# Performance work log

Hardware: AMD Instinct MI355X
Metric: run time of the kernel (lower is better)

The kernel has to match this reference:

```python
import jax, jax.numpy as jnp
import numpy as np

NUM_QUBITS = 512
NUM_CORES = 16
CORE_SIZE = 64
HIDDEN = 128
BATCH = 2048


def setup_inputs() -> dict:
    key = jax.random.key(0)
    k1, k2, k3 = jax.random.split(key, 3)
    last_assignment = jax.random.randint(k1, (BATCH, NUM_QUBITS), 0, NUM_CORES, dtype=jnp.int32)
    adjacency = jnp.ones((NUM_CORES, NUM_CORES), dtype=jnp.float32)  # all-to-all core graph
    qubit_embedding = jax.random.normal(k2, (NUM_QUBITS + 1, HIDDEN), dtype=jnp.float32)
    gcn_weight = jax.random.normal(k3, (HIDDEN, HIDDEN), dtype=jnp.float32) * (1.0 / np.sqrt(HIDDEN))
    gcn_bias = jnp.zeros((HIDDEN,), dtype=jnp.float32)
    return {
        'last_assignment': last_assignment,
        'adjacency': adjacency,
        'qubit_embedding': qubit_embedding,
        'gcn_weight': gcn_weight,
        'gcn_bias': gcn_bias,
    }


def reference(last_assignment, adjacency, qubit_embedding, gcn_weight, gcn_bias):
    B, Q = last_assignment.shape
    C = adjacency.shape[0]
    # --- replace the sequential per-qubit scatter loop with a single cumsum ---
    # pos[b,q] = number of earlier qubits assigned to the same core (the loop's
    # running counter idx); core index C (the extra row) always writes slot 0
    # because the loop resets its counter every iteration.
    oh = jax.nn.one_hot(last_assignment, C + 1, dtype=jnp.int32)        # [B,Q,C+1]
    cnt = jnp.cumsum(oh, axis=1)                                        # inclusive counts
    pos = jnp.take_along_axis(cnt, last_assignment[..., None], axis=2)[..., 0] - 1
    pos = jnp.where(last_assignment == C, 0, pos)
    buf = jnp.full((B, C + 1, CORE_SIZE), Q, dtype=jnp.int32)           # padding id = num_qubits
    b_idx = jnp.arange(B)[:, None]
    q_idx = jnp.broadcast_to(jnp.arange(Q, dtype=jnp.int32)[None, :], (B, Q))
    buf = buf.at[b_idx, last_assignment, pos].set(q_idx, mode='drop')
    buf = buf[:, :C, :]                                                 # drop overflow core row
    # --- embedding (padding row forced to zero, as nn.Embedding padding_idx) ---
    tbl = qubit_embedding.at[Q].set(0.0)
    qubit_embs = tbl[buf]                                               # [B,C,core_size,H]
    core_embs = qubit_embs.max(axis=2)                                  # [B,C,H]
    # --- GCNConv(add_self_loops=False): D^{-1/2} A D^{-1/2} (X W^T) + b ---
    deg = adjacency.sum(axis=0)
    dinv = jnp.where(deg > 0, 1.0 / jnp.sqrt(deg), 0.0)
    a_norm = adjacency * dinv[:, None] * dinv[None, :]                  # symmetric norm
    h = jnp.einsum('bch,oh->bco', core_embs, gcn_weight)                # lin (PyG: x @ W^T)
    out = jnp.einsum('ij,bjo->bio', a_norm, h) + gcn_bias               # [B,C,H]
    return out
```

## Files before the change

kernel.cpp:

```cpp
#include <hip/hip_runtime.h>
#include <stdint.h>

typedef unsigned short u16;
typedef unsigned int u32;
typedef unsigned long long u64;

typedef __bf16 bf16x8 __attribute__((ext_vector_type(8)));
typedef float f32x4 __attribute__((ext_vector_type(4)));
typedef u16 u16x8 __attribute__((ext_vector_type(8)));

#define NQ 512
#define NC 16
#define NH 128
#define NB 2048
#define ESTRIDE 136
#define HSTRIDE 24
#define QE_KEYS (513*128)
#define WT_OFF  QE_KEYS
#define GW_ELEMS (128*128)

static __device__ __forceinline__ u16 f2bf_rne(float f){
  u32 u = __float_as_uint(f);
  u += 0x7fffu + ((u>>16)&1u);
  return (u16)(u>>16);
}
static __device__ __forceinline__ u32 pack_rne(float lo, float hi){
  return (u32)f2bf_rne(lo) | ((u32)f2bf_rne(hi)<<16);
}
static __device__ __forceinline__ u16 key_of(float f){
  u16 b = f2bf_rne(f);
  return (b & 0x8000u) ? (u16)~b : (u16)(b | 0x8000u);
}
static __device__ __forceinline__ u16 unkey(u16 k){
  return (k & 0x8000u) ? (u16)(k ^ 0x8000u) : (u16)~k;
}

union Frag { u32 u[4]; uint4 u4; bf16x8 f; };
union U8   { u16x8 v; int w[4]; uint4 u4; u16 h[8]; };

__global__ void prepass_kernel(const float* __restrict__ qe,
                               const float* __restrict__ gw,
                               u16* __restrict__ ws)
{
  int idx = blockIdx.x * 256 + threadIdx.x;
  if (idx < QE_KEYS/8) {
    int i8 = idx * 8;
    uint4 o;
    if (i8 >= 512*NH) {
      o.x = 0x80008000u; o.y = 0x80008000u; o.z = 0x80008000u; o.w = 0x80008000u;
    } else {
      const float4* p = (const float4*)(qe + i8);
      float4 a = p[0], b = p[1];
      o.x = (u32)key_of(a.x) | ((u32)key_of(a.y)<<16);
      o.y = (u32)key_of(a.z) | ((u32)key_of(a.w)<<16);
      o.z = (u32)key_of(b.x) | ((u32)key_of(b.y)<<16);
      o.w = (u32)key_of(b.z) | ((u32)key_of(b.w)<<16);
    }
    *(uint4*)(ws + i8) = o;
  } else if (idx < QE_KEYS/8 + GW_ELEMS/8) {
    int j8 = (idx - QE_KEYS/8) * 8;
    const float4* p = (const float4*)(gw + j8);
    float4 a = p[0], b = p[1];
    uint4 o;
    o.x = pack_rne(a.x, a.y); o.y = pack_rne(a.z, a.w);
    o.z = pack_rne(b.x, b.y); o.w = pack_rne(b.z, b.w);
    *(uint4*)(ws + WT_OFF + j8) = o;
  }
}

__global__ __launch_bounds__(256, 8)
void core_snapshot_kernel(const int* __restrict__ la,
                          const float* __restrict__ adj,
                          const u16* __restrict__ ws,
                          const float* __restrict__ gb,
                          float* __restrict__ outp)
{
  __shared__ __align__(16) u16 sE[16*ESTRIDE];
  __shared__ __align__(16) u16 sHB[128*HSTRIDE];
  __shared__ u16 sList[16*64];
  __shared__ u32 sHist[8*16];
  __shared__ u32 sBase[8*16];
  __shared__ u32 sCnt[16];
  __shared__ float sDinv[16];

  const int tid  = threadIdx.x;
  const int lane = tid & 63;
  const int wv   = tid >> 6;
  const int m    = lane & 15;
  const int quad = lane >> 4;
  const int b    = blockIdx.x;
  const u16* qt  = ws;
  const u16* wt  = ws + WT_OFF;

  int av[2]; u32 intra[2];
  const u64 lmask = (1ull << lane) - 1ull;
  #pragma unroll
  for (int r = 0; r < 2; ++r) {
    int ch = wv*2 + r;
    av[r] = la[b*NQ + ch*64 + lane];
  }
  #pragma unroll
  for (int r = 0; r < 2; ++r) {
    int ch = wv*2 + r;
    #pragma unroll
    for (int c = 0; c < 16; ++c) {
      u64 mk = __ballot(av[r] == c);
      if (lane == c)  sHist[ch*16 + c] = (u32)__popcll(mk);
      if (av[r] == c) intra[r] = (u32)__popcll(mk & lmask);
    }
  }
  if (tid < 16) {
    float s = 0.f;
    for (int i = 0; i < 16; ++i) s += adj[i*16 + tid];
    sDinv[tid] = (s > 0.f) ? (1.0f / sqrtf(s)) : 0.f;
  }
  __syncthreads();
  if (tid < 16) {
    u32 run = 0;
    #pragma unroll
    for (int ch = 0; ch < 8; ++ch) { sBase[ch*16 + tid] = run; run += sHist[ch*16 + tid]; }
    sCnt[tid] = run;
  }
  __syncthreads();
  #pragma unroll
  for (int r = 0; r < 2; ++r) {
    int ch = wv*2 + r;
    u32 rank = sBase[ch*16 + av[r]] + intra[r];
    if (rank < 64) sList[av[r]*64 + rank] = (u16)(ch*64 + lane);
  }
  __syncthreads();

  for (int cc = 0; cc < 4; ++cc) {
    int c = wv*4 + cc;
    int cntc = (int)min(sCnt[c], 64u);
    U8 A; A.v = (u16x8)0;
    int iters = (cntc + 3) >> 2;
    for (int k = 0; k < iters; ++k) {
      int slot = k*4 + quad;
      int qv = (slot < cntc) ? (int)sList[c*64 + slot] : 512;
      U8 T; T.u4 = *(const uint4*)(qt + qv*NH + m*8);
      A.v = __builtin_elementwise_max(A.v, T.v);
    }
    U8 Bv;
    #pragma unroll
    for (int j = 0; j < 4; ++j) Bv.w[j] = __shfl_xor(A.w[j], 16);
    A.v = __builtin_elementwise_max(A.v, Bv.v);
    #pragma unroll
    for (int j = 0; j < 4; ++j) Bv.w[j] = __shfl_xor(A.w[j], 32);
    A.v = __builtin_elementwise_max(A.v, Bv.v);
    if (cntc < 64) {
      U8 Z; Z.v = (u16x8)(u16)0x8000u;
      A.v = __builtin_elementwise_max(A.v, Z.v);
    }
    if (quad == 0) {
      uint4 e;
      e.x = (u32)unkey(A.h[0]) | ((u32)unkey(A.h[1])<<16);
      e.y = (u32)unkey(A.h[2]) | ((u32)unkey(A.h[3])<<16);
      e.z = (u32)unkey(A.h[4]) | ((u32)unkey(A.h[5])<<16);
      e.w = (u32)unkey(A.h[6]) | ((u32)unkey(A.h[7])<<16);
      *(uint4*)&sE[c*ESTRIDE + m*8] = e;
    }
  }
  __syncthreads();

  {
    bf16x8 af[4];
    #pragma unroll
    for (int ks = 0; ks < 4; ++ks)
      af[ks] = *(const bf16x8*)&sE[m*ESTRIDE + ks*32 + quad*8];
    #pragma unroll
    for (int t = 0; t < 2; ++t) {
      int o = (wv*2 + t)*16 + m;
      f32x4 acc = {0.f, 0.f, 0.f, 0.f};
      #pragma unroll
      for (int ks = 0; ks < 4; ++ks) {
        bf16x8 bfr = *(const bf16x8*)(wt + o*NH + ks*32 + quad*8);
        acc = __builtin_amdgcn_mfma_f32_16x16x32_bf16(af[ks], bfr, acc, 0, 0, 0);
      }
      *(u32*)&sHB[o*HSTRIDE + quad*4]     = pack_rne(acc[0], acc[1]);
      *(u32*)&sHB[o*HSTRIDE + quad*4 + 2] = pack_rne(acc[2], acc[3]);
    }
  }
  __syncthreads();

  Frag afr2;
  #pragma unroll
  for (int jj = 0; jj < 4; ++jj) {
    float lo = 0.f, hi = 0.f;
    if (quad < 2) {
      int k0 = quad*8 + jj*2;
      lo = adj[m*16 + k0]     * sDinv[m] * sDinv[k0];
      hi = adj[m*16 + k0 + 1] * sDinv[m] * sDinv[k0 + 1];
    }
    afr2.u[jj] = pack_rne(lo, hi);
  }
  #pragma unroll
  for (int t = 0; t < 2; ++t) {
    int o = (wv*2 + t)*16 + m;
    float biasv = gb[(wv*2 + t)*16 + m];
    Frag bfr;
    if (quad < 2) bfr.u4 = *(const uint4*)&sHB[o*HSTRIDE + quad*8];
    else { bfr.u[0]=0; bfr.u[1]=0; bfr.u[2]=0; bfr.u[3]=0; }
    f32x4 acc = {biasv, biasv, biasv, biasv};
    acc = __builtin_amdgcn_mfma_f32_16x16x32_bf16(afr2.f, bfr.f, acc, 0, 0, 0);
    float* op = outp + b*(NC*NH) + o;
    #pragma unroll
    for (int r = 0; r < 4; ++r) op[(quad*4 + r)*NH] = acc[r];
  }
}

extern "C" void kernel_launch(void* const* d_in, const int* in_sizes, int n_in,
                              void* d_out, int out_size, void* d_ws, size_t ws_size,
                              hipStream_t stream) {
  const int*   la  = (const int*)d_in[0];
  const float* adj = (const float*)d_in[1];
  const float* qe  = (const float*)d_in[2];
  const float* gw  = (const float*)d_in[3];
  const float* gb  = (const float*)d_in[4];
  float* outp = (float*)d_out;
  u16* ws = (u16*)d_ws;

  int pre_threads = QE_KEYS/8 + GW_ELEMS/8;
  prepass_kernel<<<(pre_threads + 255)/256, 256, 0, stream>>>(qe, gw, ws);
  core_snapshot_kernel<<<NB, 256, 0, stream>>>(la, adj, ws, gb, outp);
}
```

Baseline: 93.92 us.

## Restructure embedding gather with transposed slot lists and two-core interleaved loads

Stores each core's qubit list transposed and pre-filled with the padding id, so each quad fetches its slot indices with vector LDS loads. The per-core max-gather becomes an unrolled loop that works on two cores at once to raise memory-level parallelism. Launch bounds drop from 8 to 6 waves per SIMD to give more registers. However, every wave now loops over all 16 cores instead of its own 4, so the embedding gather is done four times per block, which adds redundant memory traffic.

```diff
diff --git a/kernel.cpp b/kernel.cpp
--- a/kernel.cpp
+++ b/kernel.cpp
@@ -68,7 +68,17 @@
   }
 }
 
-__global__ __launch_bounds__(256, 8)
+static __device__ __forceinline__ void wave_reduce_max(U8& A){
+  U8 B;
+  #pragma unroll
+  for (int j = 0; j < 4; ++j) B.w[j] = __shfl_xor(A.w[j], 16);
+  A.v = __builtin_elementwise_max(A.v, B.v);
+  #pragma unroll
+  for (int j = 0; j < 4; ++j) B.w[j] = __shfl_xor(A.w[j], 32);
+  A.v = __builtin_elementwise_max(A.v, B.v);
+}
+
+__global__ __launch_bounds__(256, 6)
 void core_snapshot_kernel(const int* __restrict__ la,
                           const float* __restrict__ adj,
                           const u16* __restrict__ ws,
@@ -77,7 +87,7 @@
 {
   __shared__ __align__(16) u16 sE[16*ESTRIDE];
   __shared__ __align__(16) u16 sHB[128*HSTRIDE];
-  __shared__ u16 sList[16*64];
+  __shared__ __align__(16) u16 sList[16*64];
   __shared__ u32 sHist[8*16];
   __shared__ u32 sBase[8*16];
   __shared__ u32 sCnt[16];
@@ -92,6 +102,8 @@
   const u16* qt  = ws;
   const u16* wt  = ws + WT_OFF;
 
+  ((uint2*)sList)[tid] = make_uint2(0x02000200u, 0x02000200u);
+
   int av[2]; u32 intra[2];
   const u64 lmask = (1ull << lane) - 1ull;
   #pragma unroll
@@ -126,39 +138,55 @@
   for (int r = 0; r < 2; ++r) {
     int ch = wv*2 + r;
     u32 rank = sBase[ch*16 + av[r]] + intra[r];
-    if (rank < 64) sList[av[r]*64 + rank] = (u16)(ch*64 + lane);
-  }
-  __syncthreads();
-
-  for (int cc = 0; cc < 4; ++cc) {
-    int c = wv*4 + cc;
-    int cntc = (int)min(sCnt[c], 64u);
-    U8 A; A.v = (u16x8)0;
-    int iters = (cntc + 3) >> 2;
-    for (int k = 0; k < iters; ++k) {
-      int slot = k*4 + quad;
-      int qv = (slot < cntc) ? (int)sList[c*64 + slot] : 512;
-      U8 T; T.u4 = *(const uint4*)(qt + qv*NH + m*8);
-      A.v = __builtin_elementwise_max(A.v, T.v);
-    }
-    U8 Bv;
-    #pragma unroll
-    for (int j = 0; j < 4; ++j) Bv.w[j] = __shfl_xor(A.w[j], 16);
-    A.v = __builtin_elementwise_max(A.v, Bv.v);
-    #pragma unroll
-    for (int j = 0; j < 4; ++j) Bv.w[j] = __shfl_xor(A.w[j], 32);
-    A.v = __builtin_elementwise_max(A.v, Bv.v);
-    if (cntc < 64) {
+    if (rank < 64) sList[av[r]*64 + (rank&3)*16 + (rank>>2)] = (u16)(ch*64 + lane);
+  }
+  __syncthreads();
+
+  {
+    const u16* qb = qt + m*8;
+    for (int c = 0; c < 16; c += 2) {
+      U8 S0a, S0b, S1a, S1b;
+      S0a.u4 = *(const uint4*)&sList[ c   *64 + quad*16];
+      S0b.u4 = *(const uint4*)&sList[ c   *64 + quad*16 + 8];
+      S1a.u4 = *(const uint4*)&sList[(c+1)*64 + quad*16];
+      S1b.u4 = *(const uint4*)&sList[(c+1)*64 + quad*16 + 8];
+      int k0 = ((int)min(sCnt[c],   64u) + 3) >> 2;
+      int k1 = ((int)min(sCnt[c+1], 64u) + 3) >> 2;
+      U8 A0, A1; A0.v = (u16x8)0; A1.v = (u16x8)0;
+      #pragma unroll
+      for (int k = 0; k < 8; ++k) {
+        if (k < k0) { U8 T; T.u4 = *(const uint4*)(qb + (int)S0a.h[k]*NH);
+                      A0.v = __builtin_elementwise_max(A0.v, T.v); }
+        if (k < k1) { U8 T; T.u4 = *(const uint4*)(qb + (int)S1a.h[k]*NH);
+                      A1.v = __builtin_elementwise_max(A1.v, T.v); }
+      }
+      if (k0 > 8 || k1 > 8) {
+        #pragma unroll
+        for (int k = 8; k < 16; ++k) {
+          if (k < k0) { U8 T; T.u4 = *(const uint4*)(qb + (int)S0b.h[k-8]*NH);
+                        A0.v = __builtin_elementwise_max(A0.v, T.v); }
+          if (k < k1) { U8 T; T.u4 = *(const uint4*)(qb + (int)S1b.h[k-8]*NH);
+                        A1.v = __builtin_elementwise_max(A1.v, T.v); }
+        }
+      }
+      wave_reduce_max(A0);
+      wave_reduce_max(A1);
       U8 Z; Z.v = (u16x8)(u16)0x8000u;
-      A.v = __builtin_elementwise_max(A.v, Z.v);
-    }
-    if (quad == 0) {
-      uint4 e;
-      e.x = (u32)unkey(A.h[0]) | ((u32)unkey(A.h[1])<<16);
-      e.y = (u32)unkey(A.h[2]) | ((u32)unkey(A.h[3])<<16);
-      e.z = (u32)unkey(A.h[4]) | ((u32)unkey(A.h[5])<<16);
-      e.w = (u32)unkey(A.h[6]) | ((u32)unkey(A.h[7])<<16);
-      *(uint4*)&sE[c*ESTRIDE + m*8] = e;
+      if ((int)sCnt[c]   < 64) A0.v = __builtin_elementwise_max(A0.v, Z.v);
+      if ((int)sCnt[c+1] < 64) A1.v = __builtin_elementwise_max(A1.v, Z.v);
+      if (quad == 0) {
+        uint4 e;
+        e.x = (u32)unkey(A0.h[0]) | ((u32)unkey(A0.h[1])<<16);
+        e.y = (u32)unkey(A0.h[2]) | ((u32)unkey(A0.h[3])<<16);
+        e.z = (u32)unkey(A0.h[4]) | ((u32)unkey(A0.h[5])<<16);
+        e.w = (u32)unkey(A0.h[6]) | ((u32)unkey(A0.h[7])<<16);
+        *(uint4*)&sE[c*ESTRIDE + m*8] = e;
+        e.x = (u32)unkey(A1.h[0]) | ((u32)unkey(A1.h[1])<<16);
+        e.y = (u32)unkey(A1.h[2]) | ((u32)unkey(A1.h[3])<<16);
+        e.z = (u32)unkey(A1.h[4]) | ((u32)unkey(A1.h[5])<<16);
+        e.w = (u32)unkey(A1.h[6]) | ((u32)unkey(A1.h[7])<<16);
+        *(uint4*)&sE[(c+1)*ESTRIDE + m*8] = e;
+      }
     }
   }
   __syncthreads();
```

New measurement: 130.7 us. 39.2% more time.

## Batch embedding gathers for two cores with transposed slot list and padding prefill

Applied to the files above, without the earlier changes.

The slot list is prefilled with the padding id and stored transposed, so each lane group reads its qubit ids with vector LDS loads. The max-pooling gather then processes two cores at once and issues eight independent global loads before reducing, skipping the upper 32 slots when a core holds 32 or fewer qubits. This targets the serial, latency-bound loop of dependent LDS-then-global loads. Launch bounds are relaxed to allow more registers for the in-flight loads, which may lower occupancy.

```diff
diff --git a/kernel.cpp b/kernel.cpp
--- a/kernel.cpp
+++ b/kernel.cpp
@@ -68,7 +68,17 @@
   }
 }
 
-__global__ __launch_bounds__(256, 8)
+static __device__ __forceinline__ void wave_reduce_max(U8& A){
+  U8 B;
+  #pragma unroll
+  for (int j = 0; j < 4; ++j) B.w[j] = __shfl_xor(A.w[j], 16);
+  A.v = __builtin_elementwise_max(A.v, B.v);
+  #pragma unroll
+  for (int j = 0; j < 4; ++j) B.w[j] = __shfl_xor(A.w[j], 32);
+  A.v = __builtin_elementwise_max(A.v, B.v);
+}
+
+__global__ __launch_bounds__(256, 4)
 void core_snapshot_kernel(const int* __restrict__ la,
                           const float* __restrict__ adj,
                           const u16* __restrict__ ws,
@@ -77,7 +87,7 @@
 {
   __shared__ __align__(16) u16 sE[16*ESTRIDE];
   __shared__ __align__(16) u16 sHB[128*HSTRIDE];
-  __shared__ u16 sList[16*64];
+  __shared__ __align__(16) u16 sList[16*64];
   __shared__ u32 sHist[8*16];
   __shared__ u32 sBase[8*16];
   __shared__ u32 sCnt[16];
@@ -92,6 +102,8 @@
   const u16* qt  = ws;
   const u16* wt  = ws + WT_OFF;
 
+  ((uint2*)sList)[tid] = make_uint2(0x02000200u, 0x02000200u);
+
   int av[2]; u32 intra[2];
   const u64 lmask = (1ull << lane) - 1ull;
   #pragma unroll
@@ -126,39 +138,77 @@
   for (int r = 0; r < 2; ++r) {
     int ch = wv*2 + r;
     u32 rank = sBase[ch*16 + av[r]] + intra[r];
-    if (rank < 64) sList[av[r]*64 + rank] = (u16)(ch*64 + lane);
-  }
-  __syncthreads();
-
-  for (int cc = 0; cc < 4; ++cc) {
-    int c = wv*4 + cc;
-    int cntc = (int)min(sCnt[c], 64u);
-    U8 A; A.v = (u16x8)0;
-    int iters = (cntc + 3) >> 2;
-    for (int k = 0; k < iters; ++k) {
-      int slot = k*4 + quad;
-      int qv = (slot < cntc) ? (int)sList[c*64 + slot] : 512;
-      U8 T; T.u4 = *(const uint4*)(qt + qv*NH + m*8);
-      A.v = __builtin_elementwise_max(A.v, T.v);
-    }
-    U8 Bv;
-    #pragma unroll
-    for (int j = 0; j < 4; ++j) Bv.w[j] = __shfl_xor(A.w[j], 16);
-    A.v = __builtin_elementwise_max(A.v, Bv.v);
-    #pragma unroll
-    for (int j = 0; j < 4; ++j) Bv.w[j] = __shfl_xor(A.w[j], 32);
-    A.v = __builtin_elementwise_max(A.v, Bv.v);
-    if (cntc < 64) {
+    if (rank < 64) sList[av[r]*64 + (rank&3)*16 + (rank>>2)] = (u16)(ch*64 + lane);
+  }
+  __syncthreads();
+
+  {
+    const u16* qb = qt + m*8;
+    #pragma unroll
+    for (int half = 0; half < 2; ++half) {
+      const int ca = wv*4 + half*2, cb = ca + 1;
+      U8 Sa0, Sa1, Sb0, Sb1;
+      Sa0.u4 = *(const uint4*)&sList[ca*64 + quad*16];
+      Sa1.u4 = *(const uint4*)&sList[ca*64 + quad*16 + 8];
+      Sb0.u4 = *(const uint4*)&sList[cb*64 + quad*16];
+      Sb1.u4 = *(const uint4*)&sList[cb*64 + quad*16 + 8];
+      const int cna = (int)sCnt[ca], cnb = (int)sCnt[cb];
+      U8 A, B; A.v = (u16x8)0; B.v = (u16x8)0;
+      {
+        U8 Ta[4], Tb[4];
+        #pragma unroll
+        for (int k = 0; k < 4; ++k) {
+          Ta[k].u4 = *(const uint4*)(qb + (int)Sa0.h[k]*NH);
+          Tb[k].u4 = *(const uint4*)(qb + (int)Sb0.h[k]*NH);
+        }
+        #pragma unroll
+        for (int k = 0; k < 4; ++k) {
+          A.v = __builtin_elementwise_max(A.v, Ta[k].v);
+          B.v = __builtin_elementwise_max(B.v, Tb[k].v);
+        }
+        #pragma unroll
+        for (int k = 0; k < 4; ++k) {
+          Ta[k].u4 = *(const uint4*)(qb + (int)Sa0.h[k+4]*NH);
+          Tb[k].u4 = *(const uint4*)(qb + (int)Sb0.h[k+4]*NH);
+        }
+        #pragma unroll
+        for (int k = 0; k < 4; ++k) {
+          A.v = __builtin_elementwise_max(A.v, Ta[k].v);
+          B.v = __builtin_elementwise_max(B.v, Tb[k].v);
+        }
+      }
+      if (cna > 32) {
+        U8 Ta[8];
+        #pragma unroll
+        for (int k = 0; k < 8; ++k) Ta[k].u4 = *(const uint4*)(qb + (int)Sa1.h[k]*NH);
+        #pragma unroll
+        for (int k = 0; k < 8; ++k) A.v = __builtin_elementwise_max(A.v, Ta[k].v);
+      }
+      if (cnb > 32) {
+        U8 Tb[8];
+        #pragma unroll
+        for (int k = 0; k < 8; ++k) Tb[k].u4 = *(const uint4*)(qb + (int)Sb1.h[k]*NH);
+        #pragma unroll
+        for (int k = 0; k < 8; ++k) B.v = __builtin_elementwise_max(B.v, Tb[k].v);
+      }
+      wave_reduce_max(A);
+      wave_reduce_max(B);
       U8 Z; Z.v = (u16x8)(u16)0x8000u;
-      A.v = __builtin_elementwise_max(A.v, Z.v);
-    }
-    if (quad == 0) {
-      uint4 e;
-      e.x = (u32)unkey(A.h[0]) | ((u32)unkey(A.h[1])<<16);
-      e.y = (u32)unkey(A.h[2]) | ((u32)unkey(A.h[3])<<16);
-      e.z = (u32)unkey(A.h[4]) | ((u32)unkey(A.h[5])<<16);
-      e.w = (u32)unkey(A.h[6]) | ((u32)unkey(A.h[7])<<16);
-      *(uint4*)&sE[c*ESTRIDE + m*8] = e;
+      if (cna < 64) A.v = __builtin_elementwise_max(A.v, Z.v);
+      if (cnb < 64) B.v = __builtin_elementwise_max(B.v, Z.v);
+      if (quad == 0) {
+        uint4 e;
+        e.x = (u32)unkey(A.h[0]) | ((u32)unkey(A.h[1])<<16);
+        e.y = (u32)unkey(A.h[2]) | ((u32)unkey(A.h[3])<<16);
+        e.z = (u32)unkey(A.h[4]) | ((u32)unkey(A.h[5])<<16);
+        e.w = (u32)unkey(A.h[6]) | ((u32)unkey(A.h[7])<<16);
+        *(uint4*)&sE[ca*ESTRIDE + m*8] = e;
+        e.x = (u32)unkey(B.h[0]) | ((u32)unkey(B.h[1])<<16);
+        e.y = (u32)unkey(B.h[2]) | ((u32)unkey(B.h[3])<<16);
+        e.z = (u32)unkey(B.h[4]) | ((u32)unkey(B.h[5])<<16);
+        e.w = (u32)unkey(B.h[6]) | ((u32)unkey(B.h[7])<<16);
+        *(uint4*)&sE[cb*ESTRIDE + m*8] = e;
+      }
     }
   }
   __syncthreads();
```

Measured after the change: 94.70 us. About the same (+0.8%).

## Process one batch item per wavefront to remove block barriers

Applied to the files above, without the earlier changes.

Each wavefront now handles a whole batch item, so a block of four waves covers four items. This removes all __syncthreads by keeping the histogram/prefix in registers via shuffles. The normalized adjacency is precomputed once in the prepass, and the per-core gather is unrolled into 8 or 16 independent loads using a pre-padded, transposed slot list. The second MFMA's B operand is built with shuffles instead of an LDS round trip. In exchange each wave does more serial work (16 cores, 8 output tiles), and the grid shrinks to 512 blocks with lower occupancy bounds, which may reduce latency hiding.

```diff
diff --git a/kernel.cpp b/kernel.cpp
--- a/kernel.cpp
+++ b/kernel.cpp
@@ -13,11 +13,13 @@
 #define NC 16
 #define NH 128
 #define NB 2048
-#define ESTRIDE 136
-#define HSTRIDE 24
 #define QE_KEYS (513*128)
 #define WT_OFF  QE_KEYS
 #define GW_ELEMS (128*128)
+#define A_OFF (WT_OFF + GW_ELEMS)
+#define LSEG 1088
+#define ESEG 2304
+#define ESTRIDE 136
 
 static __device__ __forceinline__ u16 f2bf_rne(float f){
   u32 u = __float_as_uint(f);
@@ -40,9 +42,25 @@
 
 __global__ void prepass_kernel(const float* __restrict__ qe,
                                const float* __restrict__ gw,
+                               const float* __restrict__ adj,
                                u16* __restrict__ ws)
 {
-  int idx = blockIdx.x * 256 + threadIdx.x;
+  if (blockIdx.x == 0) {
+    __shared__ float sD[16];
+    int t = threadIdx.x;
+    if (t < 16) {
+      float s = 0.f;
+      for (int i = 0; i < 16; ++i) s += adj[i*16 + t];
+      sD[t] = (s > 0.f) ? (1.0f / sqrtf(s)) : 0.f;
+    }
+    __syncthreads();
+    int i = t >> 4, jp = (t & 15) * 2;
+    float lo = (jp   < 16) ? adj[i*16 + jp]   * sD[i] * sD[jp]   : 0.f;
+    float hi = (jp+1 < 16) ? adj[i*16 + jp+1] * sD[i] * sD[jp+1] : 0.f;
+    ((u32*)(ws + A_OFF))[t] = pack_rne(lo, hi);
+    return;
+  }
+  int idx = (blockIdx.x - 1) * 256 + threadIdx.x;
   if (idx < QE_KEYS/8) {
     int i8 = idx * 8;
     uint4 o;
@@ -68,87 +86,86 @@
   }
 }
 
-__global__ __launch_bounds__(256, 8)
+static __device__ __forceinline__ void wave_reduce_max(U8& A){
+  U8 B;
+  #pragma unroll
+  for (int j = 0; j < 4; ++j) B.w[j] = __shfl_xor(A.w[j], 16);
+  A.v = __builtin_elementwise_max(A.v, B.v);
+  #pragma unroll
+  for (int j = 0; j < 4; ++j) B.w[j] = __shfl_xor(A.w[j], 32);
+  A.v = __builtin_elementwise_max(A.v, B.v);
+}
+
+__global__ __launch_bounds__(256, 4)
 void core_snapshot_kernel(const int* __restrict__ la,
-                          const float* __restrict__ adj,
                           const u16* __restrict__ ws,
                           const float* __restrict__ gb,
                           float* __restrict__ outp)
 {
-  __shared__ __align__(16) u16 sE[16*ESTRIDE];
-  __shared__ __align__(16) u16 sHB[128*HSTRIDE];
-  __shared__ u16 sList[16*64];
-  __shared__ u32 sHist[8*16];
-  __shared__ u32 sBase[8*16];
-  __shared__ u32 sCnt[16];
-  __shared__ float sDinv[16];
+  __shared__ __align__(16) u16 sListAll[4*LSEG];
+  __shared__ __align__(16) u16 sEAll[4*ESEG];
 
   const int tid  = threadIdx.x;
   const int lane = tid & 63;
   const int wv   = tid >> 6;
   const int m    = lane & 15;
   const int quad = lane >> 4;
-  const int b    = blockIdx.x;
-  const u16* qt  = ws;
-  const u16* wt  = ws + WT_OFF;
-
-  int av[2]; u32 intra[2];
+  const int item = blockIdx.x*4 + wv;
+  u16* sList = sListAll + wv*LSEG;
+  u16* sE    = sEAll    + wv*ESEG;
+  const u16* qt = ws;
+  const u16* wt = ws + WT_OFF;
+
+  {
+    uint4 f = make_uint4(0x02000200u,0x02000200u,0x02000200u,0x02000200u);
+    *(uint4*)&sList[lane*16]     = f;
+    *(uint4*)&sList[lane*16 + 8] = f;
+  }
+
+  int av[8];
+  #pragma unroll
+  for (int ch = 0; ch < 8; ++ch) av[ch] = la[item*NQ + ch*64 + lane];
   const u64 lmask = (1ull << lane) - 1ull;
-  #pragma unroll
-  for (int r = 0; r < 2; ++r) {
-    int ch = wv*2 + r;
-    av[r] = la[b*NQ + ch*64 + lane];
-  }
-  #pragma unroll
-  for (int r = 0; r < 2; ++r) {
-    int ch = wv*2 + r;
+  u32 runbase = 0;
+  #pragma unroll
+  for (int ch = 0; ch < 8; ++ch) {
+    u32 cnt = 0, intra = 0;
     #pragma unroll
     for (int c = 0; c < 16; ++c) {
-      u64 mk = __ballot(av[r] == c);
-      if (lane == c)  sHist[ch*16 + c] = (u32)__popcll(mk);
-      if (av[r] == c) intra[r] = (u32)__popcll(mk & lmask);
-    }
-  }
-  if (tid < 16) {
-    float s = 0.f;
-    for (int i = 0; i < 16; ++i) s += adj[i*16 + tid];
-    sDinv[tid] = (s > 0.f) ? (1.0f / sqrtf(s)) : 0.f;
-  }
-  __syncthreads();
-  if (tid < 16) {
-    u32 run = 0;
-    #pragma unroll
-    for (int ch = 0; ch < 8; ++ch) { sBase[ch*16 + tid] = run; run += sHist[ch*16 + tid]; }
-    sCnt[tid] = run;
-  }
-  __syncthreads();
-  #pragma unroll
-  for (int r = 0; r < 2; ++r) {
-    int ch = wv*2 + r;
-    u32 rank = sBase[ch*16 + av[r]] + intra[r];
-    if (rank < 64) sList[av[r]*64 + rank] = (u16)(ch*64 + lane);
-  }
-  __syncthreads();
-
-  for (int cc = 0; cc < 4; ++cc) {
-    int c = wv*4 + cc;
-    int cntc = (int)min(sCnt[c], 64u);
+      u64 mk = __ballot(av[ch] == c);
+      if (lane == c)    cnt   = (u32)__popcll(mk);
+      if (av[ch] == c)  intra = (u32)__popcll(mk & lmask);
+    }
+    u32 base = (u32)__shfl((int)runbase, av[ch]);
+    u32 rank = base + intra;
+    if (rank < 64) sList[av[ch]*64 + (rank&3)*16 + (rank>>2)] = (u16)(ch*64 + lane);
+    runbase += cnt;
+  }
+  const u32 cntv = runbase;
+
+  const u16* qb = qt + m*8;
+  for (int c = 0; c < 16; ++c) {
+    int cnt = __shfl((int)cntv, c);
+    U8 S0, S1;
+    S0.u4 = *(const uint4*)&sList[c*64 + quad*16];
+    S1.u4 = *(const uint4*)&sList[c*64 + quad*16 + 8];
     U8 A; A.v = (u16x8)0;
-    int iters = (cntc + 3) >> 2;
-    for (int k = 0; k < iters; ++k) {
-      int slot = k*4 + quad;
-      int qv = (slot < cntc) ? (int)sList[c*64 + slot] : 512;
-      U8 T; T.u4 = *(const uint4*)(qt + qv*NH + m*8);
-      A.v = __builtin_elementwise_max(A.v, T.v);
-    }
-    U8 Bv;
-    #pragma unroll
-    for (int j = 0; j < 4; ++j) Bv.w[j] = __shfl_xor(A.w[j], 16);
-    A.v = __builtin_elementwise_max(A.v, Bv.v);
-    #pragma unroll
-    for (int j = 0; j < 4; ++j) Bv.w[j] = __shfl_xor(A.w[j], 32);
-    A.v = __builtin_elementwise_max(A.v, Bv.v);
-    if (cntc < 64) {
+    {
+      U8 T[8];
+      #pragma unroll
+      for (int k = 0; k < 8; ++k) T[k].u4 = *(const uint4*)(qb + (int)S0.h[k]*NH);
+      #pragma unroll
+      for (int k = 0; k < 8; ++k) A.v = __builtin_elementwise_max(A.v, T[k].v);
+    }
+    if (cnt > 32) {
+      U8 T[8];
+      #pragma unroll
+      for (int k = 0; k < 8; ++k) T[k].u4 = *(const uint4*)(qb + (int)S1.h[k]*NH);
+      #pragma unroll
+      for (int k = 0; k < 8; ++k) A.v = __builtin_elementwise_max(A.v, T[k].v);
+    }
+    wave_reduce_max(A);
+    if (cnt < 64) {
       U8 Z; Z.v = (u16x8)(u16)0x8000u;
       A.v = __builtin_elementwise_max(A.v, Z.v);
     }
@@ -161,51 +178,43 @@
       *(uint4*)&sE[c*ESTRIDE + m*8] = e;
     }
   }
-  __syncthreads();
-
-  {
-    bf16x8 af[4];
-    #pragma unroll
-    for (int ks = 0; ks < 4; ++ks)
-      af[ks] = *(const bf16x8*)&sE[m*ESTRIDE + ks*32 + quad*8];
-    #pragma unroll
-    for (int t = 0; t < 2; ++t) {
-      int o = (wv*2 + t)*16 + m;
-      f32x4 acc = {0.f, 0.f, 0.f, 0.f};
-      #pragma unroll
-      for (int ks = 0; ks < 4; ++ks) {
-        bf16x8 bfr = *(const bf16x8*)(wt + o*NH + ks*32 + quad*8);
-        acc = __builtin_amdgcn_mfma_f32_16x16x32_bf16(af[ks], bfr, acc, 0, 0, 0);
-      }
-      *(u32*)&sHB[o*HSTRIDE + quad*4]     = pack_rne(acc[0], acc[1]);
-      *(u32*)&sHB[o*HSTRIDE + quad*4 + 2] = pack_rne(acc[2], acc[3]);
-    }
-  }
-  __syncthreads();
-
-  Frag afr2;
-  #pragma unroll
-  for (int jj = 0; jj < 4; ++jj) {
-    float lo = 0.f, hi = 0.f;
-    if (quad < 2) {
-      int k0 = quad*8 + jj*2;
-      lo = adj[m*16 + k0]     * sDinv[m] * sDinv[k0];
-      hi = adj[m*16 + k0 + 1] * sDinv[m] * sDinv[k0 + 1];
-    }
-    afr2.u[jj] = pack_rne(lo, hi);
-  }
-  #pragma unroll
-  for (int t = 0; t < 2; ++t) {
-    int o = (wv*2 + t)*16 + m;
-    float biasv = gb[(wv*2 + t)*16 + m];
-    Frag bfr;
-    if (quad < 2) bfr.u4 = *(const uint4*)&sHB[o*HSTRIDE + quad*8];
-    else { bfr.u[0]=0; bfr.u[1]=0; bfr.u[2]=0; bfr.u[3]=0; }
-    f32x4 acc = {biasv, biasv, biasv, biasv};
-    acc = __builtin_amdgcn_mfma_f32_16x16x32_bf16(afr2.f, bfr.f, acc, 0, 0, 0);
-    float* op = outp + b*(NC*NH) + o;
-    #pragma unroll
-    for (int r = 0; r < 4; ++r) op[(quad*4 + r)*NH] = acc[r];
+
+  bf16x8 af[4];
+  #pragma unroll
+  for (int ks = 0; ks < 4; ++ks)
+    af[ks] = *(const bf16x8*)&sE[m*ESTRIDE + ks*32 + quad*8];
+  Frag anf;
+  anf.u4 = *(const uint4*)(ws + A_OFF + m*32 + quad*8);
+
+  #pragma unroll
+  for (int t = 0; t < 8; ++t) {
+    f32x4 acc = {0.f, 0.f, 0.f, 0.f};
+    #pragma unroll
+    for (int ks = 0; ks < 4; ++ks) {
+      bf16x8 bfr = *(const bf16x8*)(wt + (t*16 + m)*NH + ks*32 + quad*8);
+      acc = __builtin_amdgcn_mfma_f32_16x16x32_bf16(af[ks], bfr, acc, 0, 0, 0);
+    }
+    float d16[4], d32[4], lo[4], hi[4];
+    #pragma unroll
+    for (int r = 0; r < 4; ++r) {
+      d16[r] = __shfl_down(acc[r], 16);
+      d32[r] = __shfl_down(acc[r], 32);
+    }
+    #pragma unroll
+    for (int r = 0; r < 4; ++r) {
+      lo[r] = (quad == 0) ? acc[r] : d16[r];
+      hi[r] = (quad == 0) ? d16[r] : d32[r];
+    }
+    Frag hb;
+    hb.u[0] = pack_rne(lo[0], lo[1]); hb.u[1] = pack_rne(lo[2], lo[3]);
+    hb.u[2] = pack_rne(hi[0], hi[1]); hb.u[3] = pack_rne(hi[2], hi[3]);
+    if (quad >= 2) { hb.u[0]=0; hb.u[1]=0; hb.u[2]=0; hb.u[3]=0; }
+    float biasv = gb[t*16 + m];
+    f32x4 o4 = {biasv, biasv, biasv, biasv};
+    o4 = __builtin_amdgcn_mfma_f32_16x16x32_bf16(anf.f, hb.f, o4, 0, 0, 0);
+    float* op = outp + item*(NC*NH) + t*16 + m;
+    #pragma unroll
+    for (int r = 0; r < 4; ++r) op[(quad*4 + r)*NH] = o4[r];
   }
 }
 
@@ -220,7 +229,7 @@
   float* outp = (float*)d_out;
   u16* ws = (u16*)d_ws;
 
-  int pre_threads = QE_KEYS/8 + GW_ELEMS/8;
-  prepass_kernel<<<(pre_threads + 255)/256, 256, 0, stream>>>(qe, gw, ws);
-  core_snapshot_kernel<<<NB, 256, 0, stream>>>(la, adj, ws, gb, outp);
-}
+  int pre_blocks = 1 + (QE_KEYS/8 + GW_ELEMS/8 + 255)/256;
+  prepass_kernel<<<pre_blocks, 256, 0, stream>>>(qe, gw, adj, ws);
+  core_snapshot_kernel<<<NB/4, 256, 0, stream>>>(la, ws, gb, outp);
+}
```

Result: no change. 92.74 us, median of 2 (-1.3%).
